# Kernel tuning notes

Measured on AMD Instinct MI355X. Metric: run time of the kernel, lower is better.

Reference implementation:

```python
import jax, jax.numpy as jnp
import numpy as np

B, T, D, H, OUT = 1024, 512, 6, 128, 8


def setup_inputs() -> dict:
    key = jax.random.key(0)
    ks = jax.random.split(key, 24)
    n = lambda k, shp, s=0.05: jax.random.normal(k, shp, dtype=jnp.float32) * s
    return {
        "src": jax.random.normal(ks[0], (B, T, D), dtype=jnp.float32),
        # pointwise conv stack (kernel size 1 -> plain matmuls)
        "w0": n(ks[1], (H, D)), "b0": n(ks[2], (H,)),
        "w1": n(ks[3], (H, H)), "b1": n(ks[4], (H,)),
        "w2": n(ks[5], (H, H)), "b2": n(ks[6], (H,)),
        "w3": n(ks[7], (H, H)), "b3": n(ks[8], (H,)),
        "pos_embed": n(ks[9], (T, 1, H)),
        # LSTM layer 0 (PyTorch gate order i,f,g,o stacked along dim 0)
        "Wih0": n(ks[10], (4 * H, H)), "Whh0": n(ks[11], (4 * H, H)),
        "bih0": n(ks[12], (4 * H,)), "bhh0": n(ks[13], (4 * H,)),
        # LSTM layer 1
        "Wih1": n(ks[14], (4 * H, H)), "Whh1": n(ks[15], (4 * H, H)),
        "bih1": n(ks[16], (4 * H,)), "bhh1": n(ks[17], (4 * H,)),
        # head: LayerNorm + Linear(H, H//4) + GELU + Linear(H//4, OUT)
        "ln_g": jnp.ones((H,), jnp.float32), "ln_b": jnp.zeros((H,), jnp.float32),
        "hw1": n(ks[18], (H // 4, H)), "hb1": n(ks[19], (H // 4,)),
        "hw2": n(ks[20], (OUT, H // 4)), "hb2": n(ks[21], (OUT,)),
    }


def _gelu(x):
    return jax.nn.gelu(x, approximate=False)  # torch default GELU (erf)


def _lstm_layer(xs, Wih, Whh, bih, bhh):
    # xs: (T, B, H) time-major; returns (all hidden states, final hidden state)
    Hd = Whh.shape[1]
    Bd = xs.shape[1]
    bias = bih + bhh
    h0 = jnp.zeros((Bd, Hd), xs.dtype)
    c0 = jnp.zeros((Bd, Hd), xs.dtype)

    def step(carry, x):
        h, c = carry
        z = x @ Wih.T + h @ Whh.T + bias  # (B, 4H)
        i, f, g, o = jnp.split(z, 4, axis=-1)
        c = jax.nn.sigmoid(f) * c + jax.nn.sigmoid(i) * jnp.tanh(g)
        h = jax.nn.sigmoid(o) * jnp.tanh(c)
        return (h, c), h

    (h, _), ys = jax.lax.scan(step, (h0, c0), xs)
    return ys, h


def reference(src, w0, b0, w1, b1, w2, b2, w3, b3, pos_embed,
              Wih0, Whh0, bih0, bhh0, Wih1, Whh1, bih1, bhh1,
              ln_g, ln_b, hw1, hb1, hw2, hb2):
    # pointwise Conv1d+GELU stack (kernel=1 -> per-timestep matmul), eval mode
    x = _gelu(src @ w0.T + b0)            # (B, T, H)
    x = _gelu(x @ w1.T + b1)
    x = _gelu(x @ w2.T + b2)
    x = _gelu(x @ w3.T + b3)
    x = jnp.transpose(x, (1, 0, 2)) + pos_embed  # (T, B, H), broadcast pos over batch
    ys, _ = _lstm_layer(x, Wih0, Whh0, bih0, bhh0)
    _, h = _lstm_layer(ys, Wih1, Whh1, bih1, bhh1)  # final hidden of last layer, (B, H)
    # head: LayerNorm (eps=1e-5) -> Linear -> GELU -> Linear (dropout inactive in eval)
    mu = h.mean(-1, keepdims=True)
    var = ((h - mu) ** 2).mean(-1, keepdims=True)
    hn = (h - mu) * jax.lax.rsqrt(var + 1e-5) * ln_g + ln_b
    return _gelu(hn @ hw1.T + hb1) @ hw2.T + hb2  # (B, OUT)
```

## Files before the change

### kernel.cpp

```cpp
#include <hip/hip_runtime.h>
#include <hip/hip_bf16.h>
#include <cstdint>

#define T_ 512
#define B_ 1024
#define D_ 6
#define H_ 128
#define CH_ 8

typedef _Float16 f16;
typedef _Float16 f16x8 __attribute__((ext_vector_type(8)));
typedef float f32x4 __attribute__((ext_vector_type(4)));

__device__ __forceinline__ float erf_f(float x) {
    float ax = fabsf(x);
    float t = __builtin_amdgcn_rcpf(fmaf(0.3275911f, ax, 1.f));
    float p = fmaf(t, 1.061405429f, -1.453152027f);
    p = fmaf(t, p, 1.421413741f);
    p = fmaf(t, p, -0.284496736f);
    p = fmaf(t, p, 0.254829592f);
    p = p * t;
    float e = __builtin_amdgcn_exp2f(-ax * ax * 1.4426950408889634f);
    float r = 1.f - p * e;
    return copysignf(r, x);
}
__device__ __forceinline__ float gelu_f(float x) {
    return 0.5f * x * (1.f + erf_f(x * 0.7071067811865476f));
}
__device__ __forceinline__ float sig_f(float x) {
    return __builtin_amdgcn_rcpf(1.f + __builtin_amdgcn_exp2f(-1.4426950408889634f * x));
}
__device__ __forceinline__ float tanh_f(float x) {
    return 2.f * sig_f(2.f * x) - 1.f;
}
__device__ __forceinline__ f16x8 load8cvt(const float* p) {
    float4 a = ((const float4*)p)[0];
    float4 b = ((const float4*)p)[1];
    f16x8 r = { (f16)a.x, (f16)a.y, (f16)a.z, (f16)a.w,
                (f16)b.x, (f16)b.y, (f16)b.z, (f16)b.w };
    return r;
}
__device__ __forceinline__ f16x8 lds_rd8(const f16* base, int row, int cb) {
    const char* p = (const char*)base + row * 256 + (cb ^ ((row & 7) << 4));
    return *(const f16x8*)p;
}
__device__ __forceinline__ void lds_wr1(f16* base, int row, int col, f16 v) {
    char* p = (char*)base + row * 256 + ((col * 2) ^ ((row & 7) << 4));
    *(f16*)p = v;
}
__device__ __forceinline__ void zx_wr(f16* base, int row, int col, f16 v) {
    char* p = (char*)base + row * 1024 + ((col * 2) ^ ((row & 7) << 4));
    *(f16*)p = v;
}
__device__ __forceinline__ float zx_rd(const f16* base, int row, int col) {
    const char* p = (const char*)base + row * 1024 + ((col * 2) ^ ((row & 7) << 4));
    return (float)*(const f16*)p;
}

__global__ __launch_bounds__(512) void fused_conv_lstm0_k(
    const float* __restrict__ src,
    const float* __restrict__ w0p, const float* __restrict__ b0p,
    const float* __restrict__ w1p, const float* __restrict__ b1p,
    const float* __restrict__ w2p, const float* __restrict__ b2p,
    const float* __restrict__ w3p, const float* __restrict__ b3p,
    const float* __restrict__ posp,
    const float* __restrict__ Wih, const float* __restrict__ Whh,
    const float* __restrict__ bih, const float* __restrict__ bhh,
    f16* __restrict__ ys)
{
    __shared__ f16 CW[3 * 8 * 4 * 512];
    __shared__ f16 XA0[32 * 128];
    __shared__ f16 XA1[32 * 128];
    __shared__ f16 ZX[32 * 512];
    __shared__ f16 YH[32 * 128];
    __shared__ f16 HL[2][4 * 128];

    const int tid = threadIdx.x;
    const int lane = tid & 63, wid = tid >> 6;
    const int l16 = lane & 15, hi = lane >> 4;
    const int bb0 = blockIdx.x * 4;
    const int mycol = wid * 16 + l16;

    f16x8 whh[4][4];
    float biasg[4];
#pragma unroll
    for (int g = 0; g < 4; ++g) {
        int n = g * 128 + mycol;
        biasg[g] = bih[n] + bhh[n];
#pragma unroll
        for (int ki = 0; ki < 4; ++ki)
            whh[g][ki] = load8cvt(Whh + n * 128 + ki * 32 + hi * 8);
    }

    const int col0 = tid & 127;
    const int r0 = tid >> 7;
    float w0c[6], b0c;
#pragma unroll
    for (int k = 0; k < 6; ++k) w0c[k] = w0p[col0 * 6 + k];
    b0c = b0p[col0];
    const float b1c = b1p[mycol], b2c = b2p[mycol], b3c = b3p[mycol];

    {
        const float* wp[3] = { w1p, w2p, w3p };
        for (int i = tid; i < 6144; i += 512) {
            int ln = i & 63, ki = (i >> 6) & 3, cg = (i >> 8) & 7, L = i >> 11;
            f16x8 v = load8cvt(wp[L] + (cg * 16 + (ln & 15)) * 128 + ki * 32 + (ln >> 4) * 8);
            *(f16x8*)(CW + i * 8) = v;
        }
    }
    for (int i = tid; i < 2 * 4 * 128; i += 512) ((f16*)HL)[i] = (f16)0.f;

    float c = 0.f, h = 0.f;
    __syncthreads();

    auto conv_mfma = [&](const f16* Xin, f16* Xout, int L, float bc, int t0pos) {
        f16x8 bf[4];
#pragma unroll
        for (int ki = 0; ki < 4; ++ki)
            bf[ki] = *(const f16x8*)(CW + (((L * 8 + wid) * 4 + ki) << 9) + lane * 8);
#pragma unroll
        for (int mt = 0; mt < 2; ++mt) {
            f16x8 af[4];
#pragma unroll
            for (int ki = 0; ki < 4; ++ki)
                af[ki] = lds_rd8(Xin, mt * 16 + l16, ki * 64 + hi * 16);
            f32x4 acc = { bc, bc, bc, bc };
#pragma unroll
            for (int ki = 0; ki < 4; ++ki)
                acc = __builtin_amdgcn_mfma_f32_16x16x32_f16(af[ki], bf[ki], acc, 0, 0, 0);
            float pv = 0.f;
            if (t0pos >= 0) pv = posp[(t0pos + mt * 4 + hi) * 128 + mycol];
#pragma unroll
            for (int j = 0; j < 4; ++j)
                lds_wr1(Xout, mt * 16 + hi * 4 + j, mycol, (f16)(gelu_f(acc[j]) + pv));
        }
    };

    auto flushYH = [&](int tc) {
        int tau = tid >> 4, cw = tid & 15;
        f16x8 v = lds_rd8(YH, tau, cw * 16);
        *(f16x8*)(ys + (size_t)(tc + (tau >> 2)) * (B_ * H_) +
                  (size_t)(bb0 + (tau & 3)) * H_ + cw * 8) = v;
    };

    for (int t0 = 0; t0 < T_; t0 += CH_) {
        {
            const float2* sp0 = (const float2*)src + ((size_t)(bb0 + r0) * T_ + t0) * 3;
#pragma unroll
            for (int it = 0; it < CH_; ++it) {
                float2 a = sp0[it * 3 + 0], b = sp0[it * 3 + 1], c2 = sp0[it * 3 + 2];
                float acc = b0c;
                acc = fmaf(a.x, w0c[0], acc);
                acc = fmaf(a.y, w0c[1], acc);
                acc = fmaf(b.x, w0c[2], acc);
                acc = fmaf(b.y, w0c[3], acc);
                acc = fmaf(c2.x, w0c[4], acc);
                acc = fmaf(c2.y, w0c[5], acc);
                lds_wr1(XA0, it * 4 + r0, col0, (f16)gelu_f(acc));
            }
        }
        if (t0 > 0) flushYH(t0 - CH_);
        __syncthreads();
        conv_mfma(XA0, XA1, 0, b1c, -1);
        __syncthreads();
        conv_mfma(XA1, XA0, 1, b2c, -1);
        __syncthreads();
        conv_mfma(XA0, XA1, 2, b3c, t0);
        __syncthreads();
        {
            f16x8 af[2][4];
#pragma unroll
            for (int mt = 0; mt < 2; ++mt)
#pragma unroll
                for (int ki = 0; ki < 4; ++ki)
                    af[mt][ki] = lds_rd8(XA1, mt * 16 + l16, ki * 64 + hi * 16);
#pragma unroll
            for (int nt = 0; nt < 4; ++nt) {
                const int n = wid * 64 + nt * 16 + l16;
                f16x8 bf[4];
#pragma unroll
                for (int ki = 0; ki < 4; ++ki)
                    bf[ki] = load8cvt(Wih + n * 128 + ki * 32 + hi * 8);
                f32x4 za0 = { 0.f, 0.f, 0.f, 0.f };
                f32x4 za1 = { 0.f, 0.f, 0.f, 0.f };
#pragma unroll
                for (int ki = 0; ki < 4; ++ki) {
                    za0 = __builtin_amdgcn_mfma_f32_16x16x32_f16(af[0][ki], bf[ki], za0, 0, 0, 0);
                    za1 = __builtin_amdgcn_mfma_f32_16x16x32_f16(af[1][ki], bf[ki], za1, 0, 0, 0);
                }
#pragma unroll
                for (int j = 0; j < 4; ++j) {
                    zx_wr(ZX, hi * 4 + j, wid * 64 + nt * 16 + l16, (f16)za0[j]);
                    zx_wr(ZX, 16 + hi * 4 + j, wid * 64 + nt * 16 + l16, (f16)za1[j]);
                }
                __builtin_amdgcn_sched_barrier(0);
            }
        }
        __syncthreads();
        for (int it = 0; it < CH_; ++it) {
            const int t = t0 + it;
            f16x8 ha[4];
#pragma unroll
            for (int ki = 0; ki < 4; ++ki)
                ha[ki] = lds_rd8(HL[t & 1], l16 >> 2, ki * 64 + hi * 16);
            f32x4 acc[4];
#pragma unroll
            for (int g = 0; g < 4; ++g) {
                f32x4 bv = { biasg[g], biasg[g], biasg[g], biasg[g] };
                acc[g] = bv;
            }
#pragma unroll
            for (int ki = 0; ki < 4; ++ki)
#pragma unroll
                for (int g = 0; g < 4; ++g)
                    acc[g] = __builtin_amdgcn_mfma_f32_16x16x32_f16(ha[ki], whh[g][ki], acc[g], 0, 0, 0);
            float zi = acc[0][0] + zx_rd(ZX, it * 4 + hi, 0 + mycol);
            float zf = acc[1][0] + zx_rd(ZX, it * 4 + hi, 128 + mycol);
            float zg = acc[2][0] + zx_rd(ZX, it * 4 + hi, 256 + mycol);
            float zo = acc[3][0] + zx_rd(ZX, it * 4 + hi, 384 + mycol);
            c = sig_f(zf) * c + sig_f(zi) * tanh_f(zg);
            h = sig_f(zo) * tanh_f(c);
            lds_wr1(HL[(t + 1) & 1], hi, mycol, (f16)h);
            lds_wr1(YH, it * 4 + hi, mycol, (f16)h);
            __syncthreads();
        }
    }
    flushYH(T_ - CH_);
}

__global__ __launch_bounds__(512) void lstm1_k(
    const f16* __restrict__ xb,
    const float* __restrict__ Wih, const float* __restrict__ Whh,
    const float* __restrict__ bih, const float* __restrict__ bhh,
    float* __restrict__ hfin)
{
    __shared__ f16 HL[2][16 * 128];
    const int tid = threadIdx.x;
    const int lane = tid & 63, wid = tid >> 6;
    const int l16 = lane & 15, hi = lane >> 4;
    const int bb0 = blockIdx.x * 4;

    f16x8 wih[4][4], whh[4][4];
    float bias[4];
#pragma unroll
    for (int g = 0; g < 4; ++g) {
        int n = g * 128 + wid * 16 + l16;
        bias[g] = bih[n] + bhh[n];
#pragma unroll
        for (int ki = 0; ki < 4; ++ki) {
            wih[g][ki] = load8cvt(Wih + n * 128 + ki * 32 + hi * 8);
            whh[g][ki] = load8cvt(Whh + n * 128 + ki * 32 + hi * 8);
        }
    }
    for (int i = tid; i < 2 * 16 * 128; i += 512) ((f16*)HL)[i] = (f16)0.f;

    const bool arow = (l16 & 3) == 0;
    const int brow = l16 >> 2;
    const f16* xbase = xb + (size_t)(bb0 + brow) * H_;
    const int mycol = wid * 16 + l16;
    float c = 0.f, h = 0.f;
    __syncthreads();

    f16x8 xa[4];
    const f16x8 zero8 = { 0, 0, 0, 0, 0, 0, 0, 0 };
#pragma unroll
    for (int ki = 0; ki < 4; ++ki)
        xa[ki] = arow ? *(const f16x8*)(xbase + ki * 32 + hi * 8) : zero8;

    for (int t = 0; t < T_; ++t) {
        const int tn = (t + 1 < T_) ? t + 1 : T_ - 1;
        const f16* xnp = xbase + (size_t)tn * (B_ * H_);
        f16x8 xn[4];
#pragma unroll
        for (int ki = 0; ki < 4; ++ki)
            xn[ki] = arow ? *(const f16x8*)(xnp + ki * 32 + hi * 8) : zero8;

        f16x8 ha[4];
#pragma unroll
        for (int ki = 0; ki < 4; ++ki)
            ha[ki] = lds_rd8(HL[t & 1], l16, ki * 64 + hi * 16);

        f32x4 acc[4];
#pragma unroll
        for (int g = 0; g < 4; ++g) {
            f32x4 bv = { bias[g], bias[g], bias[g], bias[g] };
            acc[g] = bv;
        }
#pragma unroll
        for (int ki = 0; ki < 4; ++ki)
#pragma unroll
            for (int g = 0; g < 4; ++g)
                acc[g] = __builtin_amdgcn_mfma_f32_16x16x32_f16(xa[ki], wih[g][ki], acc[g], 0, 0, 0);
#pragma unroll
        for (int ki = 0; ki < 4; ++ki)
#pragma unroll
            for (int g = 0; g < 4; ++g)
                acc[g] = __builtin_amdgcn_mfma_f32_16x16x32_f16(ha[ki], whh[g][ki], acc[g], 0, 0, 0);

        float zi = acc[0][0], zf = acc[1][0], zg = acc[2][0], zo = acc[3][0];
        c = sig_f(zf) * c + sig_f(zi) * tanh_f(zg);
        h = sig_f(zo) * tanh_f(c);
        lds_wr1(HL[(t + 1) & 1], hi * 4, mycol, (f16)h);

#pragma unroll
        for (int ki = 0; ki < 4; ++ki) xa[ki] = xn[ki];
        __syncthreads();
    }
    hfin[(size_t)(bb0 + hi) * H_ + mycol] = h;
}

__global__ __launch_bounds__(256) void head_k(
    const float* __restrict__ hfin,
    const float* __restrict__ lng, const float* __restrict__ lnb,
    const float* __restrict__ hw1, const float* __restrict__ hb1,
    const float* __restrict__ hw2, const float* __restrict__ hb2,
    float* __restrict__ outp)
{
    __shared__ float HN[4][128];
    __shared__ float G[4][32];
    const int tid = threadIdx.x, lane = tid & 63, wid = tid >> 6;
    const int b = blockIdx.x * 4 + wid;
    float v0 = hfin[b * 128 + lane], v1 = hfin[b * 128 + 64 + lane];
    float s = v0 + v1;
#pragma unroll
    for (int m = 1; m < 64; m <<= 1) s += __shfl_xor(s, m);
    float mu = s * (1.f / 128.f);
    float d0 = v0 - mu, d1 = v1 - mu;
    float q = d0 * d0 + d1 * d1;
#pragma unroll
    for (int m = 1; m < 64; m <<= 1) q += __shfl_xor(q, m);
    float rs = rsqrtf(q * (1.f / 128.f) + 1e-5f);
    HN[wid][lane] = d0 * rs * lng[lane] + lnb[lane];
    HN[wid][64 + lane] = d1 * rs * lng[64 + lane] + lnb[64 + lane];
    __syncthreads();
    if (tid < 128) {
        int row = tid >> 5, o = tid & 31;
        float a = hb1[o];
#pragma unroll 4
        for (int k = 0; k < 128; ++k) a = fmaf(HN[row][k], hw1[o * 128 + k], a);
        G[row][o] = gelu_f(a);
    }
    __syncthreads();
    if (tid < 32) {
        int row = tid >> 3, oo = tid & 7;
        float a = hb2[oo];
#pragma unroll
        for (int k = 0; k < 32; ++k) a = fmaf(G[row][k], hw2[oo * 32 + k], a);
        outp[(size_t)(blockIdx.x * 4 + row) * 8 + oo] = a;
    }
}

extern "C" void kernel_launch(void* const* d_in, const int* in_sizes, int n_in,
                              void* d_out, int out_size, void* d_ws, size_t ws_size,
                              hipStream_t stream) {
    (void)in_sizes; (void)n_in; (void)out_size; (void)ws_size;
    const float* src  = (const float*)d_in[0];
    const float* w0   = (const float*)d_in[1];
    const float* b0   = (const float*)d_in[2];
    const float* w1   = (const float*)d_in[3];
    const float* b1   = (const float*)d_in[4];
    const float* w2   = (const float*)d_in[5];
    const float* b2   = (const float*)d_in[6];
    const float* w3   = (const float*)d_in[7];
    const float* b3   = (const float*)d_in[8];
    const float* pos  = (const float*)d_in[9];
    const float* Wih0 = (const float*)d_in[10];
    const float* Whh0 = (const float*)d_in[11];
    const float* bih0 = (const float*)d_in[12];
    const float* bhh0 = (const float*)d_in[13];
    const float* Wih1 = (const float*)d_in[14];
    const float* Whh1 = (const float*)d_in[15];
    const float* bih1 = (const float*)d_in[16];
    const float* bhh1 = (const float*)d_in[17];
    const float* lng  = (const float*)d_in[18];
    const float* lnb  = (const float*)d_in[19];
    const float* hw1  = (const float*)d_in[20];
    const float* hb1  = (const float*)d_in[21];
    const float* hw2  = (const float*)d_in[22];
    const float* hb2  = (const float*)d_in[23];
    float* outp = (float*)d_out;

    f16* ysbuf = (f16*)d_ws;
    float* hfin = (float*)((char*)d_ws + (size_t)134217728);

    fused_conv_lstm0_k<<<dim3(256), dim3(512), 0, stream>>>(
        src, w0, b0, w1, b1, w2, b2, w3, b3, pos,
        Wih0, Whh0, bih0, bhh0, ysbuf);
    lstm1_k<<<dim3(256), dim3(512), 0, stream>>>(
        ysbuf, Wih1, Whh1, bih1, bhh1, hfin);
    head_k<<<dim3(256), dim3(256), 0, stream>>>(
        hfin, lng, lnb, hw1, hb1, hw2, hb2, outp);
}
```

Before: 1.141 ms.

## Fuse LSTM layer 1 into conv+LSTM0 kernel with chunk-lagged wavefront schedule

```diff
diff --git a/kernel.cpp b/kernel.cpp
--- a/kernel.cpp
+++ b/kernel.cpp
@@ -57,23 +57,26 @@
     return (float)*(const f16*)p;
 }
 
-__global__ __launch_bounds__(512) void fused_conv_lstm0_k(
+__global__ __launch_bounds__(512) void fused_all_k(
     const float* __restrict__ src,
     const float* __restrict__ w0p, const float* __restrict__ b0p,
     const float* __restrict__ w1p, const float* __restrict__ b1p,
     const float* __restrict__ w2p, const float* __restrict__ b2p,
     const float* __restrict__ w3p, const float* __restrict__ b3p,
     const float* __restrict__ posp,
-    const float* __restrict__ Wih, const float* __restrict__ Whh,
-    const float* __restrict__ bih, const float* __restrict__ bhh,
-    f16* __restrict__ ys)
+    const float* __restrict__ Wih0, const float* __restrict__ Whh0,
+    const float* __restrict__ bih0, const float* __restrict__ bhh0,
+    const float* __restrict__ Wih1, const float* __restrict__ Whh1,
+    const float* __restrict__ bih1, const float* __restrict__ bhh1,
+    float* __restrict__ hfin)
 {
-    __shared__ f16 CW[3 * 8 * 4 * 512];
     __shared__ f16 XA0[32 * 128];
     __shared__ f16 XA1[32 * 128];
-    __shared__ f16 ZX[32 * 512];
-    __shared__ f16 YH[32 * 128];
-    __shared__ f16 HL[2][4 * 128];
+    __shared__ f16 ZX0[32 * 512];
+    __shared__ f16 ZX1[32 * 512];
+    __shared__ f16 YH[2][32 * 128];
+    __shared__ f16 HL0[2][4 * 128];
+    __shared__ f16 HL1[2][4 * 128];
 
     const int tid = threadIdx.x;
     const int lane = tid & 63, wid = tid >> 6;
@@ -81,15 +84,18 @@
     const int bb0 = blockIdx.x * 4;
     const int mycol = wid * 16 + l16;
 
-    f16x8 whh[4][4];
-    float biasg[4];
+    f16x8 whh0[4][4], whh1[4][4];
+    float bg0[4], bg1[4];
 #pragma unroll
     for (int g = 0; g < 4; ++g) {
         int n = g * 128 + mycol;
-        biasg[g] = bih[n] + bhh[n];
-#pragma unroll
-        for (int ki = 0; ki < 4; ++ki)
-            whh[g][ki] = load8cvt(Whh + n * 128 + ki * 32 + hi * 8);
+        bg0[g] = bih0[n] + bhh0[n];
+        bg1[g] = bih1[n] + bhh1[n];
+#pragma unroll
+        for (int ki = 0; ki < 4; ++ki) {
+            whh0[g][ki] = load8cvt(Whh0 + n * 128 + ki * 32 + hi * 8);
+            whh1[g][ki] = load8cvt(Whh1 + n * 128 + ki * 32 + hi * 8);
+        }
     }
 
     const int col0 = tid & 127;
@@ -100,24 +106,19 @@
     b0c = b0p[col0];
     const float b1c = b1p[mycol], b2c = b2p[mycol], b3c = b3p[mycol];
 
-    {
-        const float* wp[3] = { w1p, w2p, w3p };
-        for (int i = tid; i < 6144; i += 512) {
-            int ln = i & 63, ki = (i >> 6) & 3, cg = (i >> 8) & 7, L = i >> 11;
-            f16x8 v = load8cvt(wp[L] + (cg * 16 + (ln & 15)) * 128 + ki * 32 + (ln >> 4) * 8);
-            *(f16x8*)(CW + i * 8) = v;
-        }
-    }
-    for (int i = tid; i < 2 * 4 * 128; i += 512) ((f16*)HL)[i] = (f16)0.f;
-
-    float c = 0.f, h = 0.f;
+    for (int i = tid; i < 2 * 4 * 128; i += 512) {
+        ((f16*)HL0)[i] = (f16)0.f;
+        ((f16*)HL1)[i] = (f16)0.f;
+    }
+
+    float c0 = 0.f, h0 = 0.f, c1 = 0.f, h1 = 0.f;
     __syncthreads();
 
-    auto conv_mfma = [&](const f16* Xin, f16* Xout, int L, float bc, int t0pos) {
+    auto conv_mfma = [&](const f16* Xin, f16* Xout, const float* Wg, float bc, int t0pos) {
         f16x8 bf[4];
 #pragma unroll
         for (int ki = 0; ki < 4; ++ki)
-            bf[ki] = *(const f16x8*)(CW + (((L * 8 + wid) * 4 + ki) << 9) + lane * 8);
+            bf[ki] = load8cvt(Wg + mycol * 128 + ki * 32 + hi * 8);
 #pragma unroll
         for (int mt = 0; mt < 2; ++mt) {
             f16x8 af[4];
@@ -136,14 +137,66 @@
         }
     };
 
-    auto flushYH = [&](int tc) {
-        int tau = tid >> 4, cw = tid & 15;
-        f16x8 v = lds_rd8(YH, tau, cw * 16);
-        *(f16x8*)(ys + (size_t)(tc + (tau >> 2)) * (B_ * H_) +
-                  (size_t)(bb0 + (tau & 3)) * H_ + cw * 8) = v;
+    auto zgemm = [&](const f16* Ain, const float* Wg, f16* ZXout) {
+        f16x8 af[2][4];
+#pragma unroll
+        for (int mt = 0; mt < 2; ++mt)
+#pragma unroll
+            for (int ki = 0; ki < 4; ++ki)
+                af[mt][ki] = lds_rd8(Ain, mt * 16 + l16, ki * 64 + hi * 16);
+#pragma unroll
+        for (int nt = 0; nt < 4; ++nt) {
+            const int n = wid * 64 + nt * 16 + l16;
+            f16x8 bf[4];
+#pragma unroll
+            for (int ki = 0; ki < 4; ++ki)
+                bf[ki] = load8cvt(Wg + n * 128 + ki * 32 + hi * 8);
+            f32x4 za0 = { 0.f, 0.f, 0.f, 0.f };
+            f32x4 za1 = { 0.f, 0.f, 0.f, 0.f };
+#pragma unroll
+            for (int ki = 0; ki < 4; ++ki) {
+                za0 = __builtin_amdgcn_mfma_f32_16x16x32_f16(af[0][ki], bf[ki], za0, 0, 0, 0);
+                za1 = __builtin_amdgcn_mfma_f32_16x16x32_f16(af[1][ki], bf[ki], za1, 0, 0, 0);
+            }
+#pragma unroll
+            for (int j = 0; j < 4; ++j) {
+                zx_wr(ZXout, hi * 4 + j, wid * 64 + nt * 16 + l16, (f16)za0[j]);
+                zx_wr(ZXout, 16 + hi * 4 + j, wid * 64 + nt * 16 + l16, (f16)za1[j]);
+            }
+            __builtin_amdgcn_sched_barrier(0);
+        }
     };
 
-    for (int t0 = 0; t0 < T_; t0 += CH_) {
+    auto lstep = [&](f16 (*HLd)[4 * 128], int t, const f16x8 (&whf)[4][4],
+                     const float (&bg)[4], const f16* ZXp, int it,
+                     float& cc, float& hh, f16* yout) {
+        f16x8 ha[4];
+#pragma unroll
+        for (int ki = 0; ki < 4; ++ki)
+            ha[ki] = lds_rd8(HLd[t & 1], l16 >> 2, ki * 64 + hi * 16);
+        f32x4 acc[4];
+#pragma unroll
+        for (int g = 0; g < 4; ++g) {
+            f32x4 bv = { bg[g], bg[g], bg[g], bg[g] };
+            acc[g] = bv;
+        }
+#pragma unroll
+        for (int ki = 0; ki < 4; ++ki)
+#pragma unroll
+            for (int g = 0; g < 4; ++g)
+                acc[g] = __builtin_amdgcn_mfma_f32_16x16x32_f16(ha[ki], whf[g][ki], acc[g], 0, 0, 0);
+        float zi = acc[0][0] + zx_rd(ZXp, it * 4 + hi, 0 + mycol);
+        float zf = acc[1][0] + zx_rd(ZXp, it * 4 + hi, 128 + mycol);
+        float zg = acc[2][0] + zx_rd(ZXp, it * 4 + hi, 256 + mycol);
+        float zo = acc[3][0] + zx_rd(ZXp, it * 4 + hi, 384 + mycol);
+        cc = sig_f(zf) * cc + sig_f(zi) * tanh_f(zg);
+        hh = sig_f(zo) * tanh_f(cc);
+        lds_wr1(HLd[(t + 1) & 1], hi, mycol, (f16)hh);
+        if (yout) lds_wr1(yout, it * 4 + hi, mycol, (f16)hh);
+    };
+
+    for (int k = 0; k < T_ / CH_; ++k) {
+        const int t0 = k * CH_;
         {
             const float2* sp0 = (const float2*)src + ((size_t)(bb0 + r0) * T_ + t0) * 3;
 #pragma unroll
@@ -159,154 +212,31 @@
                 lds_wr1(XA0, it * 4 + r0, col0, (f16)gelu_f(acc));
             }
         }
-        if (t0 > 0) flushYH(t0 - CH_);
-        __syncthreads();
-        conv_mfma(XA0, XA1, 0, b1c, -1);
-        __syncthreads();
-        conv_mfma(XA1, XA0, 1, b2c, -1);
-        __syncthreads();
-        conv_mfma(XA0, XA1, 2, b3c, t0);
-        __syncthreads();
-        {
-            f16x8 af[2][4];
-#pragma unroll
-            for (int mt = 0; mt < 2; ++mt)
-#pragma unroll
-                for (int ki = 0; ki < 4; ++ki)
-                    af[mt][ki] = lds_rd8(XA1, mt * 16 + l16, ki * 64 + hi * 16);
-#pragma unroll
-            for (int nt = 0; nt < 4; ++nt) {
-                const int n = wid * 64 + nt * 16 + l16;
-                f16x8 bf[4];
-#pragma unroll
-                for (int ki = 0; ki < 4; ++ki)
-                    bf[ki] = load8cvt(Wih + n * 128 + ki * 32 + hi * 8);
-                f32x4 za0 = { 0.f, 0.f, 0.f, 0.f };
-                f32x4 za1 = { 0.f, 0.f, 0.f, 0.f };
-#pragma unroll
-                for (int ki = 0; ki < 4; ++ki) {
-                    za0 = __builtin_amdgcn_mfma_f32_16x16x32_f16(af[0][ki], bf[ki], za0, 0, 0, 0);
-                    za1 = __builtin_amdgcn_mfma_f32_16x16x32_f16(af[1][ki], bf[ki], za1, 0, 0, 0);
-                }
-#pragma unroll
-                for (int j = 0; j < 4; ++j) {
-                    zx_wr(ZX, hi * 4 + j, wid * 64 + nt * 16 + l16, (f16)za0[j]);
-                    zx_wr(ZX, 16 + hi * 4 + j, wid * 64 + nt * 16 + l16, (f16)za1[j]);
-                }
-                __builtin_amdgcn_sched_barrier(0);
-            }
-        }
+        __syncthreads();
+        conv_mfma(XA0, XA1, w1p, b1c, -1);
+        __syncthreads();
+        conv_mfma(XA1, XA0, w2p, b2c, -1);
+        __syncthreads();
+        conv_mfma(XA0, XA1, w3p, b3c, t0);
+        __syncthreads();
+        zgemm(XA1, Wih0, ZX0);
+        if (k > 0) zgemm(YH[(k ^ 1) & 1], Wih1, ZX1);
         __syncthreads();
         for (int it = 0; it < CH_; ++it) {
             const int t = t0 + it;
-            f16x8 ha[4];
-#pragma unroll
-            for (int ki = 0; ki < 4; ++ki)
-                ha[ki] = lds_rd8(HL[t & 1], l16 >> 2, ki * 64 + hi * 16);
-            f32x4 acc[4];
-#pragma unroll
-            for (int g = 0; g < 4; ++g) {
-                f32x4 bv = { biasg[g], biasg[g], biasg[g], biasg[g] };
-                acc[g] = bv;
-            }
-#pragma unroll
-            for (int ki = 0; ki < 4; ++ki)
-#pragma unroll
-                for (int g = 0; g < 4; ++g)
-                    acc[g] = __builtin_amdgcn_mfma_f32_16x16x32_f16(ha[ki], whh[g][ki], acc[g], 0, 0, 0);
-            float zi = acc[0][0] + zx_rd(ZX, it * 4 + hi, 0 + mycol);
-            float zf = acc[1][0] + zx_rd(ZX, it * 4 + hi, 128 + mycol);
-            float zg = acc[2][0] + zx_rd(ZX, it * 4 + hi, 256 + mycol);
-            float zo = acc[3][0] + zx_rd(ZX, it * 4 + hi, 384 + mycol);
-            c = sig_f(zf) * c + sig_f(zi) * tanh_f(zg);
-            h = sig_f(zo) * tanh_f(c);
-            lds_wr1(HL[(t + 1) & 1], hi, mycol, (f16)h);
-            lds_wr1(YH, it * 4 + hi, mycol, (f16)h);
+            lstep(HL0, t, whh0, bg0, ZX0, it, c0, h0, YH[k & 1]);
+            if (k > 0) lstep(HL1, t, whh1, bg1, ZX1, it, c1, h1, nullptr);
             __syncthreads();
         }
     }
-    flushYH(T_ - CH_);
-}
-
-__global__ __launch_bounds__(512) void lstm1_k(
-    const f16* __restrict__ xb,
-    const float* __restrict__ Wih, const float* __restrict__ Whh,
-    const float* __restrict__ bih, const float* __restrict__ bhh,
-    float* __restrict__ hfin)
-{
-    __shared__ f16 HL[2][16 * 128];
-    const int tid = threadIdx.x;
-    const int lane = tid & 63, wid = tid >> 6;
-    const int l16 = lane & 15, hi = lane >> 4;
-    const int bb0 = blockIdx.x * 4;
-
-    f16x8 wih[4][4], whh[4][4];
-    float bias[4];
-#pragma unroll
-    for (int g = 0; g < 4; ++g) {
-        int n = g * 128 + wid * 16 + l16;
-        bias[g] = bih[n] + bhh[n];
-#pragma unroll
-        for (int ki = 0; ki < 4; ++ki) {
-            wih[g][ki] = load8cvt(Wih + n * 128 + ki * 32 + hi * 8);
-            whh[g][ki] = load8cvt(Whh + n * 128 + ki * 32 + hi * 8);
-        }
-    }
-    for (int i = tid; i < 2 * 16 * 128; i += 512) ((f16*)HL)[i] = (f16)0.f;
-
-    const bool arow = (l16 & 3) == 0;
-    const int brow = l16 >> 2;
-    const f16* xbase = xb + (size_t)(bb0 + brow) * H_;
-    const int mycol = wid * 16 + l16;
-    float c = 0.f, h = 0.f;
+    zgemm(YH[(T_ / CH_ - 1) & 1], Wih1, ZX1);
     __syncthreads();
-
-    f16x8 xa[4];
-    const f16x8 zero8 = { 0, 0, 0, 0, 0, 0, 0, 0 };
-#pragma unroll
-    for (int ki = 0; ki < 4; ++ki)
-        xa[ki] = arow ? *(const f16x8*)(xbase + ki * 32 + hi * 8) : zero8;
-
-    for (int t = 0; t < T_; ++t) {
-        const int tn = (t + 1 < T_) ? t + 1 : T_ - 1;
-        const f16* xnp = xbase + (size_t)tn * (B_ * H_);
-        f16x8 xn[4];
-#pragma unroll
-        for (int ki = 0; ki < 4; ++ki)
-            xn[ki] = arow ? *(const f16x8*)(xnp + ki * 32 + hi * 8) : zero8;
-
-        f16x8 ha[4];
-#pragma unroll
-        for (int ki = 0; ki < 4; ++ki)
-            ha[ki] = lds_rd8(HL[t & 1], l16, ki * 64 + hi * 16);
-
-        f32x4 acc[4];
-#pragma unroll
-        for (int g = 0; g < 4; ++g) {
-            f32x4 bv = { bias[g], bias[g], bias[g], bias[g] };
-            acc[g] = bv;
-        }
-#pragma unroll
-        for (int ki = 0; ki < 4; ++ki)
-#pragma unroll
-            for (int g = 0; g < 4; ++g)
-                acc[g] = __builtin_amdgcn_mfma_f32_16x16x32_f16(xa[ki], wih[g][ki], acc[g], 0, 0, 0);
-#pragma unroll
-        for (int ki = 0; ki < 4; ++ki)
-#pragma unroll
-            for (int g = 0; g < 4; ++g)
-                acc[g] = __builtin_amdgcn_mfma_f32_16x16x32_f16(ha[ki], whh[g][ki], acc[g], 0, 0, 0);
-
-        float zi = acc[0][0], zf = acc[1][0], zg = acc[2][0], zo = acc[3][0];
-        c = sig_f(zf) * c + sig_f(zi) * tanh_f(zg);
-        h = sig_f(zo) * tanh_f(c);
-        lds_wr1(HL[(t + 1) & 1], hi * 4, mycol, (f16)h);
-
-#pragma unroll
-        for (int ki = 0; ki < 4; ++ki) xa[ki] = xn[ki];
-        __syncthreads();
-    }
-    hfin[(size_t)(bb0 + hi) * H_ + mycol] = h;
+    for (int it = 0; it < CH_; ++it) {
+        const int t = (T_ - CH_) + it;
+        lstep(HL1, t, whh1, bg1, ZX1, it, c1, h1, nullptr);
+        __syncthreads();
+    }
+    hfin[(size_t)(bb0 + hi) * H_ + mycol] = h1;
 }
 
 __global__ __launch_bounds__(256) void head_k(
@@ -380,14 +310,11 @@
     const float* hb2  = (const float*)d_in[23];
     float* outp = (float*)d_out;
 
-    f16* ysbuf = (f16*)d_ws;
-    float* hfin = (float*)((char*)d_ws + (size_t)134217728);
-
-    fused_conv_lstm0_k<<<dim3(256), dim3(512), 0, stream>>>(
+    float* hfin = (float*)d_ws;
+
+    fused_all_k<<<dim3(256), dim3(512), 0, stream>>>(
         src, w0, b0, w1, b1, w2, b2, w3, b3, pos,
-        Wih0, Whh0, bih0, bhh0, ysbuf);
-    lstm1_k<<<dim3(256), dim3(512), 0, stream>>>(
-        ysbuf, Wih1, Whh1, bih1, bhh1, hfin);
+        Wih0, Whh0, bih0, bhh0, Wih1, Whh1, bih1, bhh1, hfin);
     head_k<<<dim3(256), dim3(256), 0, stream>>>(
         hfin, lng, lnb, hw1, hb1, hw2, hb2, outp);
 }
```

After: 2.740 ms. +140.0%, slower.

## Precompute LSTM1 input projection per 8-step chunk into LDS

Applied to the files above, without the earlier changes.

```diff
diff --git a/kernel.cpp b/kernel.cpp
--- a/kernel.cpp
+++ b/kernel.cpp
@@ -228,83 +228,97 @@
     flushYH(T_ - CH_);
 }
 
-__global__ __launch_bounds__(512) void lstm1_k(
-    const f16* __restrict__ xb,
+__global__ __launch_bounds__(512) void lstm1_chunk_k(
+    const f16* __restrict__ ys,
     const float* __restrict__ Wih, const float* __restrict__ Whh,
     const float* __restrict__ bih, const float* __restrict__ bhh,
     float* __restrict__ hfin)
 {
-    __shared__ f16 HL[2][16 * 128];
+    __shared__ f16 ZX[32 * 512];
+    __shared__ f16 HL[2][4 * 128];
+
     const int tid = threadIdx.x;
     const int lane = tid & 63, wid = tid >> 6;
     const int l16 = lane & 15, hi = lane >> 4;
     const int bb0 = blockIdx.x * 4;
-
-    f16x8 wih[4][4], whh[4][4];
-    float bias[4];
+    const int mycol = wid * 16 + l16;
+
+    f16x8 whh[4][4];
+    float biasg[4];
 #pragma unroll
     for (int g = 0; g < 4; ++g) {
-        int n = g * 128 + wid * 16 + l16;
-        bias[g] = bih[n] + bhh[n];
-#pragma unroll
-        for (int ki = 0; ki < 4; ++ki) {
-            wih[g][ki] = load8cvt(Wih + n * 128 + ki * 32 + hi * 8);
+        int n = g * 128 + mycol;
+        biasg[g] = bih[n] + bhh[n];
+#pragma unroll
+        for (int ki = 0; ki < 4; ++ki)
             whh[g][ki] = load8cvt(Whh + n * 128 + ki * 32 + hi * 8);
-        }
-    }
-    for (int i = tid; i < 2 * 16 * 128; i += 512) ((f16*)HL)[i] = (f16)0.f;
-
-    const bool arow = (l16 & 3) == 0;
-    const int brow = l16 >> 2;
-    const f16* xbase = xb + (size_t)(bb0 + brow) * H_;
-    const int mycol = wid * 16 + l16;
+    }
+    for (int i = tid; i < 2 * 4 * 128; i += 512) ((f16*)HL)[i] = (f16)0.f;
+
     float c = 0.f, h = 0.f;
     __syncthreads();
 
-    f16x8 xa[4];
-    const f16x8 zero8 = { 0, 0, 0, 0, 0, 0, 0, 0 };
-#pragma unroll
-    for (int ki = 0; ki < 4; ++ki)
-        xa[ki] = arow ? *(const f16x8*)(xbase + ki * 32 + hi * 8) : zero8;
-
-    for (int t = 0; t < T_; ++t) {
-        const int tn = (t + 1 < T_) ? t + 1 : T_ - 1;
-        const f16* xnp = xbase + (size_t)tn * (B_ * H_);
-        f16x8 xn[4];
-#pragma unroll
-        for (int ki = 0; ki < 4; ++ki)
-            xn[ki] = arow ? *(const f16x8*)(xnp + ki * 32 + hi * 8) : zero8;
-
-        f16x8 ha[4];
-#pragma unroll
-        for (int ki = 0; ki < 4; ++ki)
-            ha[ki] = lds_rd8(HL[t & 1], l16, ki * 64 + hi * 16);
-
-        f32x4 acc[4];
-#pragma unroll
-        for (int g = 0; g < 4; ++g) {
-            f32x4 bv = { bias[g], bias[g], bias[g], bias[g] };
-            acc[g] = bv;
-        }
-#pragma unroll
-        for (int ki = 0; ki < 4; ++ki)
-#pragma unroll
-            for (int g = 0; g < 4; ++g)
-                acc[g] = __builtin_amdgcn_mfma_f32_16x16x32_f16(xa[ki], wih[g][ki], acc[g], 0, 0, 0);
-#pragma unroll
-        for (int ki = 0; ki < 4; ++ki)
-#pragma unroll
-            for (int g = 0; g < 4; ++g)
-                acc[g] = __builtin_amdgcn_mfma_f32_16x16x32_f16(ha[ki], whh[g][ki], acc[g], 0, 0, 0);
-
-        float zi = acc[0][0], zf = acc[1][0], zg = acc[2][0], zo = acc[3][0];
-        c = sig_f(zf) * c + sig_f(zi) * tanh_f(zg);
-        h = sig_f(zo) * tanh_f(c);
-        lds_wr1(HL[(t + 1) & 1], hi * 4, mycol, (f16)h);
-
-#pragma unroll
-        for (int ki = 0; ki < 4; ++ki) xa[ki] = xn[ki];
-        __syncthreads();
+    for (int t0 = 0; t0 < T_; t0 += CH_) {
+        {
+            f16x8 af[2][4];
+#pragma unroll
+            for (int mt = 0; mt < 2; ++mt) {
+                const int tau = mt * 16 + l16;
+                const f16* ap = ys + (size_t)(t0 + (tau >> 2)) * (B_ * H_) +
+                                (size_t)(bb0 + (tau & 3)) * H_;
+#pragma unroll
+                for (int ki = 0; ki < 4; ++ki)
+                    af[mt][ki] = *(const f16x8*)(ap + ki * 32 + hi * 8);
+            }
+#pragma unroll
+            for (int nt = 0; nt < 4; ++nt) {
+                const int n = wid * 64 + nt * 16 + l16;
+                f16x8 bf[4];
+#pragma unroll
+                for (int ki = 0; ki < 4; ++ki)
+                    bf[ki] = load8cvt(Wih + n * 128 + ki * 32 + hi * 8);
+                f32x4 za0 = { 0.f, 0.f, 0.f, 0.f };
+                f32x4 za1 = { 0.f, 0.f, 0.f, 0.f };
+#pragma unroll
+                for (int ki = 0; ki < 4; ++ki) {
+                    za0 = __builtin_amdgcn_mfma_f32_16x16x32_f16(af[0][ki], bf[ki], za0, 0, 0, 0);
+                    za1 = __builtin_amdgcn_mfma_f32_16x16x32_f16(af[1][ki], bf[ki], za1, 0, 0, 0);
+                }
+#pragma unroll
+                for (int j = 0; j < 4; ++j) {
+                    zx_wr(ZX, hi * 4 + j, wid * 64 + nt * 16 + l16, (f16)za0[j]);
+                    zx_wr(ZX, 16 + hi * 4 + j, wid * 64 + nt * 16 + l16, (f16)za1[j]);
+                }
+                __builtin_amdgcn_sched_barrier(0);
+            }
+        }
+        __syncthreads();
+        for (int it = 0; it < CH_; ++it) {
+            const int t = t0 + it;
+            f16x8 ha[4];
+#pragma unroll
+            for (int ki = 0; ki < 4; ++ki)
+                ha[ki] = lds_rd8(HL[t & 1], l16 >> 2, ki * 64 + hi * 16);
+            f32x4 acc[4];
+#pragma unroll
+            for (int g = 0; g < 4; ++g) {
+                f32x4 bv = { biasg[g], biasg[g], biasg[g], biasg[g] };
+                acc[g] = bv;
+            }
+#pragma unroll
+            for (int ki = 0; ki < 4; ++ki)
+#pragma unroll
+                for (int g = 0; g < 4; ++g)
+                    acc[g] = __builtin_amdgcn_mfma_f32_16x16x32_f16(ha[ki], whh[g][ki], acc[g], 0, 0, 0);
+            float zi = acc[0][0] + zx_rd(ZX, it * 4 + hi, 0 + mycol);
+            float zf = acc[1][0] + zx_rd(ZX, it * 4 + hi, 128 + mycol);
+            float zg = acc[2][0] + zx_rd(ZX, it * 4 + hi, 256 + mycol);
+            float zo = acc[3][0] + zx_rd(ZX, it * 4 + hi, 384 + mycol);
+            c = sig_f(zf) * c + sig_f(zi) * tanh_f(zg);
+            h = sig_f(zo) * tanh_f(c);
+            lds_wr1(HL[(t + 1) & 1], hi, mycol, (f16)h);
+            __syncthreads();
+        }
     }
     hfin[(size_t)(bb0 + hi) * H_ + mycol] = h;
 }
@@ -386,7 +400,7 @@
     fused_conv_lstm0_k<<<dim3(256), dim3(512), 0, stream>>>(
         src, w0, b0, w1, b1, w2, b2, w3, b3, pos,
         Wih0, Whh0, bih0, bhh0, ysbuf);
-    lstm1_k<<<dim3(256), dim3(512), 0, stream>>>(
+    lstm1_chunk_k<<<dim3(256), dim3(512), 0, stream>>>(
         ysbuf, Wih1, Whh1, bih1, bhh1, hfin);
     head_k<<<dim3(256), dim3(256), 0, stream>>>(
         hfin, lng, lnb, hw1, hb1, hw2, hb2, outp);
```

New measurement: 1.092 ms. -4.4%, faster.

## Split conv stack into parallel kernel and reuse chunked LSTM kernel for both layers

Applied to the files above, without the earlier changes.

```diff
diff --git a/kernel.cpp b/kernel.cpp
--- a/kernel.cpp
+++ b/kernel.cpp
@@ -7,6 +7,7 @@
 #define D_ 6
 #define H_ 128
 #define CH_ 8
+#define CT_ 16
 
 typedef _Float16 f16;
 typedef _Float16 f16x8 __attribute__((ext_vector_type(8)));
@@ -57,20 +58,99 @@
     return (float)*(const f16*)p;
 }
 
-__global__ __launch_bounds__(512) void fused_conv_lstm0_k(
+__global__ __launch_bounds__(512) void conv_k(
     const float* __restrict__ src,
     const float* __restrict__ w0p, const float* __restrict__ b0p,
     const float* __restrict__ w1p, const float* __restrict__ b1p,
     const float* __restrict__ w2p, const float* __restrict__ b2p,
     const float* __restrict__ w3p, const float* __restrict__ b3p,
-    const float* __restrict__ posp,
+    const float* __restrict__ posp, f16* __restrict__ xout)
+{
+    __shared__ f16 XA0[64 * 128];
+    __shared__ f16 XA1[64 * 128];
+    const int tid = threadIdx.x;
+    const int lane = tid & 63, wid = tid >> 6;
+    const int l16 = lane & 15, hi = lane >> 4;
+    const int t0 = (blockIdx.x & 31) * CT_;
+    const int bb0 = (blockIdx.x >> 5) * 4;
+    const int mycol = wid * 16 + l16;
+
+    f16x8 cw[3][4];
+    {
+        const float* wp[3] = { w1p, w2p, w3p };
+#pragma unroll
+        for (int L = 0; L < 3; ++L)
+#pragma unroll
+            for (int ki = 0; ki < 4; ++ki)
+                cw[L][ki] = load8cvt(wp[L] + mycol * 128 + ki * 32 + hi * 8);
+    }
+    const int col0 = tid & 127;
+    const int r0 = tid >> 7;
+    float w0c[6], b0c;
+#pragma unroll
+    for (int k = 0; k < 6; ++k) w0c[k] = w0p[col0 * 6 + k];
+    b0c = b0p[col0];
+    const float b1c = b1p[mycol], b2c = b2p[mycol], b3c = b3p[mycol];
+
+    {
+        const float2* sp0 = (const float2*)src + ((size_t)(bb0 + r0) * T_ + t0) * 3;
+#pragma unroll
+        for (int it = 0; it < CT_; ++it) {
+            float2 a = sp0[it * 3 + 0], b = sp0[it * 3 + 1], c2 = sp0[it * 3 + 2];
+            float acc = b0c;
+            acc = fmaf(a.x, w0c[0], acc);
+            acc = fmaf(a.y, w0c[1], acc);
+            acc = fmaf(b.x, w0c[2], acc);
+            acc = fmaf(b.y, w0c[3], acc);
+            acc = fmaf(c2.x, w0c[4], acc);
+            acc = fmaf(c2.y, w0c[5], acc);
+            lds_wr1(XA0, it * 4 + r0, col0, (f16)gelu_f(acc));
+        }
+    }
+    __syncthreads();
+
+    auto conv_mfma = [&](const f16* Xin, f16* Xout, int L, float bc, bool addpos) {
+#pragma unroll
+        for (int mt = 0; mt < 4; ++mt) {
+            f16x8 af[4];
+#pragma unroll
+            for (int ki = 0; ki < 4; ++ki)
+                af[ki] = lds_rd8(Xin, mt * 16 + l16, ki * 64 + hi * 16);
+            f32x4 acc = { bc, bc, bc, bc };
+#pragma unroll
+            for (int ki = 0; ki < 4; ++ki)
+                acc = __builtin_amdgcn_mfma_f32_16x16x32_f16(af[ki], cw[L][ki], acc, 0, 0, 0);
+            float pv = 0.f;
+            if (addpos) pv = posp[(t0 + mt * 4 + hi) * 128 + mycol];
+#pragma unroll
+            for (int j = 0; j < 4; ++j)
+                lds_wr1(Xout, mt * 16 + hi * 4 + j, mycol, (f16)(gelu_f(acc[j]) + pv));
+        }
+    };
+    conv_mfma(XA0, XA1, 0, b1c, false);
+    __syncthreads();
+    conv_mfma(XA1, XA0, 1, b2c, false);
+    __syncthreads();
+    conv_mfma(XA0, XA1, 2, b3c, true);
+    __syncthreads();
+
+#pragma unroll
+    for (int pass = 0; pass < 2; ++pass) {
+        int u = pass * 512 + tid;
+        int tau = u >> 4, cw8 = u & 15;
+        f16x8 v = lds_rd8(XA1, tau, cw8 * 16);
+        *(f16x8*)(xout + (size_t)(t0 + (tau >> 2)) * (B_ * H_) +
+                  (size_t)(bb0 + (tau & 3)) * H_ + cw8 * 8) = v;
+    }
+}
+
+template <bool WRITE_YS, bool WRITE_H>
+__global__ __launch_bounds__(512) void lstm_chunk_k(
+    const f16* __restrict__ xb,
     const float* __restrict__ Wih, const float* __restrict__ Whh,
     const float* __restrict__ bih, const float* __restrict__ bhh,
-    f16* __restrict__ ys)
+    f16* __restrict__ ys, float* __restrict__ hfin)
 {
-    __shared__ f16 CW[3 * 8 * 4 * 512];
-    __shared__ f16 XA0[32 * 128];
-    __shared__ f16 XA1[32 * 128];
     __shared__ f16 ZX[32 * 512];
     __shared__ f16 YH[32 * 128];
     __shared__ f16 HL[2][4 * 128];
@@ -91,89 +171,31 @@
         for (int ki = 0; ki < 4; ++ki)
             whh[g][ki] = load8cvt(Whh + n * 128 + ki * 32 + hi * 8);
     }
-
-    const int col0 = tid & 127;
-    const int r0 = tid >> 7;
-    float w0c[6], b0c;
-#pragma unroll
-    for (int k = 0; k < 6; ++k) w0c[k] = w0p[col0 * 6 + k];
-    b0c = b0p[col0];
-    const float b1c = b1p[mycol], b2c = b2p[mycol], b3c = b3p[mycol];
-
-    {
-        const float* wp[3] = { w1p, w2p, w3p };
-        for (int i = tid; i < 6144; i += 512) {
-            int ln = i & 63, ki = (i >> 6) & 3, cg = (i >> 8) & 7, L = i >> 11;
-            f16x8 v = load8cvt(wp[L] + (cg * 16 + (ln & 15)) * 128 + ki * 32 + (ln >> 4) * 8);
-            *(f16x8*)(CW + i * 8) = v;
-        }
-    }
     for (int i = tid; i < 2 * 4 * 128; i += 512) ((f16*)HL)[i] = (f16)0.f;
 
     float c = 0.f, h = 0.f;
     __syncthreads();
 
-    auto conv_mfma = [&](const f16* Xin, f16* Xout, int L, float bc, int t0pos) {
-        f16x8 bf[4];
-#pragma unroll
-        for (int ki = 0; ki < 4; ++ki)
-            bf[ki] = *(const f16x8*)(CW + (((L * 8 + wid) * 4 + ki) << 9) + lane * 8);
-#pragma unroll
-        for (int mt = 0; mt < 2; ++mt) {
-            f16x8 af[4];
-#pragma unroll
-            for (int ki = 0; ki < 4; ++ki)
-                af[ki] = lds_rd8(Xin, mt * 16 + l16, ki * 64 + hi * 16);
-            f32x4 acc = { bc, bc, bc, bc };
-#pragma unroll
-            for (int ki = 0; ki < 4; ++ki)
-                acc = __builtin_amdgcn_mfma_f32_16x16x32_f16(af[ki], bf[ki], acc, 0, 0, 0);
-            float pv = 0.f;
-            if (t0pos >= 0) pv = posp[(t0pos + mt * 4 + hi) * 128 + mycol];
-#pragma unroll
-            for (int j = 0; j < 4; ++j)
-                lds_wr1(Xout, mt * 16 + hi * 4 + j, mycol, (f16)(gelu_f(acc[j]) + pv));
-        }
+    auto flushYH = [&](int tc) {
+        int tau = tid >> 4, cw8 = tid & 15;
+        f16x8 v = lds_rd8(YH, tau, cw8 * 16);
+        *(f16x8*)(ys + (size_t)(tc + (tau >> 2)) * (B_ * H_) +
+                  (size_t)(bb0 + (tau & 3)) * H_ + cw8 * 8) = v;
     };
 
-    auto flushYH = [&](int tc) {
-        int tau = tid >> 4, cw = tid & 15;
-        f16x8 v = lds_rd8(YH, tau, cw * 16);
-        *(f16x8*)(ys + (size_t)(tc + (tau >> 2)) * (B_ * H_) +
-                  (size_t)(bb0 + (tau & 3)) * H_ + cw * 8) = v;
-    };
-
     for (int t0 = 0; t0 < T_; t0 += CH_) {
-        {
-            const float2* sp0 = (const float2*)src + ((size_t)(bb0 + r0) * T_ + t0) * 3;
-#pragma unroll
-            for (int it = 0; it < CH_; ++it) {
-                float2 a = sp0[it * 3 + 0], b = sp0[it * 3 + 1], c2 = sp0[it * 3 + 2];
-                float acc = b0c;
-                acc = fmaf(a.x, w0c[0], acc);
-                acc = fmaf(a.y, w0c[1], acc);
-                acc = fmaf(b.x, w0c[2], acc);
-                acc = fmaf(b.y, w0c[3], acc);
-                acc = fmaf(c2.x, w0c[4], acc);
-                acc = fmaf(c2.y, w0c[5], acc);
-                lds_wr1(XA0, it * 4 + r0, col0, (f16)gelu_f(acc));
-            }
-        }
-        if (t0 > 0) flushYH(t0 - CH_);
-        __syncthreads();
-        conv_mfma(XA0, XA1, 0, b1c, -1);
-        __syncthreads();
-        conv_mfma(XA1, XA0, 1, b2c, -1);
-        __syncthreads();
-        conv_mfma(XA0, XA1, 2, b3c, t0);
-        __syncthreads();
+        if (WRITE_YS && t0 > 0) flushYH(t0 - CH_);
         {
             f16x8 af[2][4];
 #pragma unroll
-            for (int mt = 0; mt < 2; ++mt)
+            for (int mt = 0; mt < 2; ++mt) {
+                const int tau = mt * 16 + l16;
+                const f16* ap = xb + (size_t)(t0 + (tau >> 2)) * (B_ * H_) +
+                                (size_t)(bb0 + (tau & 3)) * H_;
 #pragma unroll
                 for (int ki = 0; ki < 4; ++ki)
-                    af[mt][ki] = lds_rd8(XA1, mt * 16 + l16, ki * 64 + hi * 16);
+                    af[mt][ki] = *(const f16x8*)(ap + ki * 32 + hi * 8);
+            }
 #pragma unroll
             for (int nt = 0; nt < 4; ++nt) {
                 const int n = wid * 64 + nt * 16 + l16;
@@ -221,92 +243,12 @@
             c = sig_f(zf) * c + sig_f(zi) * tanh_f(zg);
             h = sig_f(zo) * tanh_f(c);
             lds_wr1(HL[(t + 1) & 1], hi, mycol, (f16)h);
-            lds_wr1(YH, it * 4 + hi, mycol, (f16)h);
+            if (WRITE_YS) lds_wr1(YH, it * 4 + hi, mycol, (f16)h);
             __syncthreads();
         }
     }
-    flushYH(T_ - CH_);
-}
-
-__global__ __launch_bounds__(512) void lstm1_k(
-    const f16* __restrict__ xb,
-    const float* __restrict__ Wih, const float* __restrict__ Whh,
-    const float* __restrict__ bih, const float* __restrict__ bhh,
-    float* __restrict__ hfin)
-{
-    __shared__ f16 HL[2][16 * 128];
-    const int tid = threadIdx.x;
-    const int lane = tid & 63, wid = tid >> 6;
-    const int l16 = lane & 15, hi = lane >> 4;
-    const int bb0 = blockIdx.x * 4;
-
-    f16x8 wih[4][4], whh[4][4];
-    float bias[4];
-#pragma unroll
-    for (int g = 0; g < 4; ++g) {
-        int n = g * 128 + wid * 16 + l16;
-        bias[g] = bih[n] + bhh[n];
-#pragma unroll
-        for (int ki = 0; ki < 4; ++ki) {
-            wih[g][ki] = load8cvt(Wih + n * 128 + ki * 32 + hi * 8);
-            whh[g][ki] = load8cvt(Whh + n * 128 + ki * 32 + hi * 8);
-        }
-    }
-    for (int i = tid; i < 2 * 16 * 128; i += 512) ((f16*)HL)[i] = (f16)0.f;
-
-    const bool arow = (l16 & 3) == 0;
-    const int brow = l16 >> 2;
-    const f16* xbase = xb + (size_t)(bb0 + brow) * H_;
-    const int mycol = wid * 16 + l16;
-    float c = 0.f, h = 0.f;
-    __syncthreads();
-
-    f16x8 xa[4];
-    const f16x8 zero8 = { 0, 0, 0, 0, 0, 0, 0, 0 };
-#pragma unroll
-    for (int ki = 0; ki < 4; ++ki)
-        xa[ki] = arow ? *(const f16x8*)(xbase + ki * 32 + hi * 8) : zero8;
-
-    for (int t = 0; t < T_; ++t) {
-        const int tn = (t + 1 < T_) ? t + 1 : T_ - 1;
-        const f16* xnp = xbase + (size_t)tn * (B_ * H_);
-        f16x8 xn[4];
-#pragma unroll
-        for (int ki = 0; ki < 4; ++ki)
-            xn[ki] = arow ? *(const f16x8*)(xnp + ki * 32 + hi * 8) : zero8;
-
-        f16x8 ha[4];
-#pragma unroll
-        for (int ki = 0; ki < 4; ++ki)
-            ha[ki] = lds_rd8(HL[t & 1], l16, ki * 64 + hi * 16);
-
-        f32x4 acc[4];
-#pragma unroll
-        for (int g = 0; g < 4; ++g) {
-            f32x4 bv = { bias[g], bias[g], bias[g], bias[g] };
-            acc[g] = bv;
-        }
-#pragma unroll
-        for (int ki = 0; ki < 4; ++ki)
-#pragma unroll
-            for (int g = 0; g < 4; ++g)
-                acc[g] = __builtin_amdgcn_mfma_f32_16x16x32_f16(xa[ki], wih[g][ki], acc[g], 0, 0, 0);
-#pragma unroll
-        for (int ki = 0; ki < 4; ++ki)
-#pragma unroll
-            for (int g = 0; g < 4; ++g)
-                acc[g] = __builtin_amdgcn_mfma_f32_16x16x32_f16(ha[ki], whh[g][ki], acc[g], 0, 0, 0);
-
-        float zi = acc[0][0], zf = acc[1][0], zg = acc[2][0], zo = acc[3][0];
-        c = sig_f(zf) * c + sig_f(zi) * tanh_f(zg);
-        h = sig_f(zo) * tanh_f(c);
-        lds_wr1(HL[(t + 1) & 1], hi * 4, mycol, (f16)h);
-
-#pragma unroll
-        for (int ki = 0; ki < 4; ++ki) xa[ki] = xn[ki];
-        __syncthreads();
-    }
-    hfin[(size_t)(bb0 + hi) * H_ + mycol] = h;
+    if (WRITE_YS) flushYH(T_ - CH_);
+    if (WRITE_H) hfin[(size_t)(bb0 + hi) * H_ + mycol] = h;
 }
 
 __global__ __launch_bounds__(256) void head_k(
@@ -380,14 +322,15 @@
     const float* hb2  = (const float*)d_in[23];
     float* outp = (float*)d_out;
 
-    f16* ysbuf = (f16*)d_ws;
+    f16* xbuf = (f16*)d_ws;
     float* hfin = (float*)((char*)d_ws + (size_t)134217728);
 
-    fused_conv_lstm0_k<<<dim3(256), dim3(512), 0, stream>>>(
-        src, w0, b0, w1, b1, w2, b2, w3, b3, pos,
-        Wih0, Whh0, bih0, bhh0, ysbuf);
-    lstm1_k<<<dim3(256), dim3(512), 0, stream>>>(
-        ysbuf, Wih1, Whh1, bih1, bhh1, hfin);
+    conv_k<<<dim3(8192), dim3(512), 0, stream>>>(
+        src, w0, b0, w1, b1, w2, b2, w3, b3, pos, xbuf);
+    lstm_chunk_k<true, false><<<dim3(256), dim3(512), 0, stream>>>(
+        xbuf, Wih0, Whh0, bih0, bhh0, xbuf, nullptr);
+    lstm_chunk_k<false, true><<<dim3(256), dim3(512), 0, stream>>>(
+        xbuf, Wih1, Whh1, bih1, bhh1, nullptr, hfin);
     head_k<<<dim3(256), dim3(256), 0, stream>>>(
         hfin, lng, lnb, hw1, hb1, hw2, hb2, outp);
 }
```

After: 1.063 ms (median of 2 runs). 6.9% less time.
